# Performance work log

Hardware: AMD Instinct MI355X
Metric: run time of the kernel (lower is better)

## Reference

```python
import jax, jax.numpy as jnp
import numpy as np

NUM_LAYERS = 2


def _lstm_scan(x, w_ih, w_hh):
    """x: [S,B,I]; w_ih: [4H,I]; w_hh: [4H,H]. Returns per-step (hs, cs): [S,B,H]."""
    S, B, _ = x.shape
    H = w_hh.shape[1]
    xg = jnp.einsum('sbi,gi->sbg', x, w_ih)  # precompute input contributions [S,B,4H]

    def step(carry, xg_t):
        h, c = carry
        gates = xg_t + h @ w_hh.T
        i, f, g, o = jnp.split(gates, 4, axis=-1)  # torch LSTM gate order
        i = jax.nn.sigmoid(i)
        f = jax.nn.sigmoid(f)
        g = jnp.tanh(g)
        o = jax.nn.sigmoid(o)
        c = f * c + i * g
        h = o * jnp.tanh(c)
        return (h, c), (h, c)

    init = (jnp.zeros((B, H), x.dtype), jnp.zeros((B, H), x.dtype))
    _, (hs, cs) = jax.lax.scan(step, init, xg)
    return hs, cs


def _stacked(x, w_ih, w_hh, reverse):
    """Stacked unidirectional LSTM. w_ih/w_hh: [L,4H,*].
    Returns (out [S,B,H], h_last [L,B,H], c_last [L,B,H]) matching stackedRNN
    semantics: for reverse, the returned 'last' hidden is the per-step state at
    original time index S-1 (first step processed in the reverse loop)."""
    h_last, c_last = [], []
    cur = x
    for layer in range(w_ih.shape[0]):
        xin = jnp.flip(cur, axis=0) if reverse else cur
        hs, cs = _lstm_scan(xin, w_ih[layer], w_hh[layer])
        if reverse:
            hs = jnp.flip(hs, axis=0)
            cs = jnp.flip(cs, axis=0)
        cur = hs
        h_last.append(hs[-1])  # faithful to torch code's layer[-1] indexing
        c_last.append(cs[-1])
    return cur, jnp.stack(h_last, 0), jnp.stack(c_last, 0)


def setup_inputs() -> dict:
    key = jax.random.key(0)
    ks = jax.random.split(key, 5)
    S, B, I, H, L = 256, 32, 1024, 1024, NUM_LAYERS
    stdev = 1.0 / np.sqrt(H)
    u = lambda k, shape: jax.random.uniform(k, shape, jnp.float32, -stdev, stdev)
    return {
        'x': jax.random.normal(ks[0], (S, B, I), jnp.float32),
        'w_ih_fwd': u(ks[1], (L, 4 * H, I)),
        'w_hh_fwd': u(ks[2], (L, 4 * H, H)),
        'w_ih_bwd': u(ks[3], (L, 4 * H, I)),
        'w_hh_bwd': u(ks[4], (L, 4 * H, H)),
    }


def reference(x, w_ih_fwd, w_hh_fwd, w_ih_bwd, w_hh_bwd):
    out_f, h_f, c_f = _stacked(x, w_ih_fwd, w_hh_fwd, reverse=False)
    out_b, h_b, c_b = _stacked(x, w_ih_bwd, w_hh_bwd, reverse=True)
    output = jnp.concatenate([out_f, out_b], axis=-1)      # [S,B,2H]
    h_all = jnp.concatenate([h_f, h_b], axis=-1)            # [L,B,2H]
    c_all = jnp.concatenate([c_f, c_b], axis=-1)            # [L,B,2H]
    return output, h_all, c_all
```

## Files before the change

### kernel.cpp

```cpp
#include <hip/hip_runtime.h>
#include <stdint.h>

#define SEQ   256
#define BSZ   32
#define HD    1024
#define GD    4096
#define KD    1024
#define MROWS (SEQ*BSZ)
#define PBLK  256
#define PTHR  512

typedef unsigned short u16;
typedef __attribute__((ext_vector_type(8))) __bf16 bf8_t;
typedef __attribute__((ext_vector_type(4))) float  f4_t;
typedef __attribute__((ext_vector_type(4))) unsigned int u4_t;

__device__ __forceinline__ u16 f2bf(float f) {
  unsigned u = __float_as_uint(f);
  u += 0x7fffu + ((u >> 16) & 1u);
  return (u16)(u >> 16);
}
__device__ __forceinline__ float sigm(float x) { return 1.0f / (1.0f + __expf(-x)); }
__device__ __forceinline__ float tanh_f(float x) {
  float e = __expf(-2.0f * x);
  return 2.0f / (1.0f + e) - 1.0f;
}

__global__ void cvt_f32_bf16(const float* __restrict__ src, u16* __restrict__ dst, int n4) {
  int i = blockIdx.x * blockDim.x + threadIdx.x;
  if (i >= n4) return;
  float4 v = ((const float4*)src)[i];
  ushort4 o;
  o.x = f2bf(v.x); o.y = f2bf(v.y); o.z = f2bf(v.z); o.w = f2bf(v.w);
  ((ushort4*)dst)[i] = o;
}

__global__ void reorder_whh(const float* __restrict__ src, u16* __restrict__ dst, int d) {
  int r = blockIdx.x;
  int layer = r >> 12, row = r & 4095;
  int g = row >> 10, j = row & 1023;
  int jblk = j >> 4, jl = j & 15;
  size_t drow = ((size_t)(d * 2 + layer) * 64 + jblk) * 64 + g * 16 + jl;
  float4 v = ((const float4*)(src + (size_t)r * KD))[threadIdx.x];
  ushort4 o;
  o.x = f2bf(v.x); o.y = f2bf(v.y); o.z = f2bf(v.z); o.w = f2bf(v.w);
  ((ushort4*)(dst + drow * KD))[threadIdx.x] = o;
}

__global__ __launch_bounds__(PTHR, 2) void lstm_persist(
    const u16* __restrict__ whh_r,
    const u16* __restrict__ wih_r,
    const u16* __restrict__ xbf,
    u16*       __restrict__ h0t,
    u16*       __restrict__ h1t,
    float*     __restrict__ dout,
    unsigned*  __restrict__ cntb)
{
  const int tid = threadIdx.x;
  const int lane = tid & 63;
  const int wv  = tid >> 6;
  const int mt = wv >> 1, kh = wv & 1;
  const int bid = blockIdx.x;
  const int layer = bid >> 7;
  const int d = bid & 1, jblk = (bid >> 1) & 63;
  const int j0 = jblk * 16;
  const int fr = lane & 15, quad = lane >> 4;
  unsigned* cnt   = cntb + (size_t)(layer * 2 + d) * 512;
  unsigned* cntbl = cntb + (size_t)d * 512;

  __builtin_amdgcn_fence(__ATOMIC_ACQUIRE, "agent");

  __shared__ __align__(16) uint32_t lX[32 * 512];
  __shared__ __align__(16) uint32_t lH[32 * 512];
  __shared__ __align__(16) float lAcc[4096];

  u16*       hme = (layer ? h1t : h0t) + (size_t)d * MROWS * HD;
  const u16* hbl = h0t + (size_t)d * MROWS * HD;

  u4_t wih[16], whh[16];
  {
    const size_t rb = ((size_t)((d * 2 + layer) * 64 + jblk) * 64 + mt * 16 + fr) * KD
                    + kh * 512 + quad * 8;
    #pragma unroll
    for (int ks = 0; ks < 16; ks++) wih[ks] = *(const u4_t*)(wih_r + rb + ks * 32);
    #pragma unroll
    for (int ks = 0; ks < 16; ks++) whh[ks] = *(const u4_t*)(whh_r + rb + ks * 32);
    #pragma unroll
    for (int ks = 0; ks < 16; ks++) {
      asm volatile("" : "+v"(wih[ks]));
      asm volatile("" : "+v"(whh[ks]));
    }
  }

  const int b_ = tid >> 3, jp = tid & 7;
  float cr0 = 0.0f, cr1 = 0.0f;

  for (int t = 0; t < SEQ; t++) {
    const int tt = d ? (SEQ - 1 - t) : t;

    if (tid == 0) {
      const unsigned go = 8u * (unsigned)t;
      const unsigned gb = 8u * (unsigned)(t + 1);
      long spins = 0;
      for (;;) {
        bool ok = (__hip_atomic_load(&cnt[0], __ATOMIC_RELAXED, __HIP_MEMORY_SCOPE_AGENT) >= go);
        if (ok && layer)
          ok = (__hip_atomic_load(&cntbl[0], __ATOMIC_RELAXED, __HIP_MEMORY_SCOPE_AGENT) >= gb);
        if (ok) break;
        if (++spins > (1L << 22)) break;
      }
    }
    __syncthreads();
    asm volatile("" ::: "memory");

    if (wv < 4) {
      if (layer) {
        const unsigned long long* s8 = (const unsigned long long*)(hbl + (size_t)tt * BSZ * HD);
        #pragma unroll
        for (int hf = 0; hf < 2; hf++) {
          unsigned long long hv2[16];
          #pragma unroll
          for (int k = 0; k < 8; k++) {
            int kk = hf * 8 + k, row = wv * 8 + (kk >> 1), c = (kk & 1) * 64 + lane;
            size_t ci = ((size_t)row * 128 + c) * 2;
            hv2[2 * k]     = __hip_atomic_load(s8 + ci,     __ATOMIC_RELAXED, __HIP_MEMORY_SCOPE_AGENT);
            hv2[2 * k + 1] = __hip_atomic_load(s8 + ci + 1, __ATOMIC_RELAXED, __HIP_MEMORY_SCOPE_AGENT);
          }
          #pragma unroll
          for (int k = 0; k < 8; k++) {
            int kk = hf * 8 + k, row = wv * 8 + (kk >> 1), c = (kk & 1) * 64 + lane;
            int pc = c ^ (row & 7);
            uint2 lo = __builtin_bit_cast(uint2, hv2[2 * k]);
            uint2 hi = __builtin_bit_cast(uint2, hv2[2 * k + 1]);
            u4_t v; v.x = lo.x; v.y = lo.y; v.z = hi.x; v.w = hi.y;
            *(u4_t*)&lX[row * 512 + pc * 4] = v;
          }
        }
      } else if (t == 0) {
        const u16* xs = xbf + (size_t)(tt * BSZ) * KD;
        #pragma unroll
        for (int k = 0; k < 16; k++) {
          int row = wv * 8 + (k >> 1), c = (k & 1) * 64 + lane, pc = c ^ (row & 7);
          u4_t v = *(const u4_t*)(xs + (size_t)row * KD + c * 8);
          *(u4_t*)&lX[row * 512 + pc * 4] = v;
        }
      }
    } else if (t > 0) {
      const int q = wv - 4;
      const int ttp = d ? (tt + 1) : (tt - 1);
      const unsigned long long* s8 = (const unsigned long long*)(hme + (size_t)ttp * BSZ * HD);
      #pragma unroll
      for (int hf = 0; hf < 2; hf++) {
        unsigned long long hv2[16];
        #pragma unroll
        for (int k = 0; k < 8; k++) {
          int kk = hf * 8 + k, row = q * 8 + (kk >> 1), c = (kk & 1) * 64 + lane;
          size_t ci = ((size_t)row * 128 + c) * 2;
          hv2[2 * k]     = __hip_atomic_load(s8 + ci,     __ATOMIC_RELAXED, __HIP_MEMORY_SCOPE_AGENT);
          hv2[2 * k + 1] = __hip_atomic_load(s8 + ci + 1, __ATOMIC_RELAXED, __HIP_MEMORY_SCOPE_AGENT);
        }
        #pragma unroll
        for (int k = 0; k < 8; k++) {
          int kk = hf * 8 + k, row = q * 8 + (kk >> 1), c = (kk & 1) * 64 + lane;
          int pc = c ^ (row & 7);
          uint2 lo = __builtin_bit_cast(uint2, hv2[2 * k]);
          uint2 hi = __builtin_bit_cast(uint2, hv2[2 * k + 1]);
          u4_t v; v.x = lo.x; v.y = lo.y; v.z = hi.x; v.w = hi.y;
          *(u4_t*)&lH[row * 512 + pc * 4] = v;
        }
      }
    }
    __syncthreads();

    f4_t acc0 = {}, acc1 = {};
    #pragma unroll
    for (int ks = 0; ks < 16; ks++) {
      int cbase = ((kh * 64 + ks * 4 + quad) ^ (fr & 7)) << 2;
      bf8_t a0 = *(const bf8_t*)&lX[fr * 512 + cbase];
      bf8_t a1 = *(const bf8_t*)&lX[(fr + 16) * 512 + cbase];
      bf8_t wb = __builtin_bit_cast(bf8_t, wih[ks]);
      acc0 = __builtin_amdgcn_mfma_f32_16x16x32_bf16(a0, wb, acc0, 0, 0, 0);
      acc1 = __builtin_amdgcn_mfma_f32_16x16x32_bf16(a1, wb, acc1, 0, 0, 0);
    }
    if (t > 0) {
      #pragma unroll
      for (int ks = 0; ks < 16; ks++) {
        int cbase = ((kh * 64 + ks * 4 + quad) ^ (fr & 7)) << 2;
        bf8_t a0 = *(const bf8_t*)&lH[fr * 512 + cbase];
        bf8_t a1 = *(const bf8_t*)&lH[(fr + 16) * 512 + cbase];
        bf8_t wb = __builtin_bit_cast(bf8_t, whh[ks]);
        acc0 = __builtin_amdgcn_mfma_f32_16x16x32_bf16(a0, wb, acc0, 0, 0, 0);
        acc1 = __builtin_amdgcn_mfma_f32_16x16x32_bf16(a1, wb, acc1, 0, 0, 0);
      }
    }
    #pragma unroll
    for (int r = 0; r < 4; r++) {
      lAcc[((mt * 2 + kh) * 32 + quad * 4 + r) * 16 + fr]      = acc0[r];
      lAcc[((mt * 2 + kh) * 32 + 16 + quad * 4 + r) * 16 + fr] = acc1[r];
    }
    __syncthreads();

    if (tid < 256) {
      float vg0[4], vg1[4];
      #pragma unroll
      for (int g = 0; g < 4; g++) {
        float2 p0 = *(const float2*)&lAcc[((g * 2 + 0) * 32 + b_) * 16 + 2 * jp];
        float2 p1 = *(const float2*)&lAcc[((g * 2 + 1) * 32 + b_) * 16 + 2 * jp];
        vg0[g] = p0.x + p1.x;
        vg1[g] = p0.y + p1.y;
      }
      float i0 = sigm(vg0[0]), f0 = sigm(vg0[1]), g0 = tanh_f(vg0[2]), o0 = sigm(vg0[3]);
      float i1 = sigm(vg1[0]), f1 = sigm(vg1[1]), g1 = tanh_f(vg1[2]), o1 = sigm(vg1[3]);
      cr0 = f0 * cr0 + i0 * g0;
      cr1 = f1 * cr1 + i1 * g1;
      float hn0 = o0 * tanh_f(cr0), hn1 = o1 * tanh_f(cr1);
      uint32_t hnp = ((uint32_t)f2bf(hn1) << 16) | (uint32_t)f2bf(hn0);

      size_t hq = (((size_t)tt * BSZ + b_) * HD + j0 + 2 * jp) >> 1;
      __hip_atomic_store((uint32_t*)hme + hq, hnp, __ATOMIC_RELAXED, __HIP_MEMORY_SCOPE_AGENT);

      if (layer == 1) {
        float2 o2 = make_float2(hn0, hn1);
        *(float2*)&dout[((size_t)tt * BSZ + b_) * (2 * HD) + (size_t)d * HD + j0 + 2 * jp] = o2;
      }
      if ((d == 0 && t == SEQ - 1) || (d == 1 && t == 0)) {
        size_t hoff = (size_t)MROWS * 2 * HD + ((size_t)layer * BSZ + b_) * (2 * HD)
                    + (size_t)d * HD + j0 + 2 * jp;
        dout[hoff] = hn0;  dout[hoff + 1] = hn1;
        dout[hoff + (size_t)2 * BSZ * 2 * HD]     = cr0;
        dout[hoff + (size_t)2 * BSZ * 2 * HD + 1] = cr1;
      }
      asm volatile("s_waitcnt vmcnt(0)" ::: "memory");
    }

    if (!layer && wv < 4 && t + 1 < SEQ) {
      const int ttn = d ? (SEQ - 2 - t) : (t + 1);
      const u16* xs = xbf + (size_t)(ttn * BSZ) * KD;
      #pragma unroll
      for (int k = 0; k < 16; k++) {
        int row = wv * 8 + (k >> 1), c = (k & 1) * 64 + lane, pc = c ^ (row & 7);
        u4_t v = *(const u4_t*)(xs + (size_t)row * KD + c * 8);
        *(u4_t*)&lX[row * 512 + pc * 4] = v;
      }
    }

    __syncthreads();
    if (tid == 0) {
      const unsigned sub = (unsigned)(jblk & 7);
      unsigned old = __hip_atomic_fetch_add(&cnt[16 * (1 + sub)], 1u,
                                            __ATOMIC_RELAXED, __HIP_MEMORY_SCOPE_AGENT);
      if (old + 1u == 8u * (unsigned)(t + 1))
        __hip_atomic_fetch_add(&cnt[0], 1u, __ATOMIC_RELAXED, __HIP_MEMORY_SCOPE_AGENT);
    }
  }
}

extern "C" void kernel_launch(void* const* d_in, const int* in_sizes, int n_in,
                              void* d_out, int out_size, void* d_ws, size_t ws_size,
                              hipStream_t stream) {
  const float* x    = (const float*)d_in[0];
  const float* wihf = (const float*)d_in[1];
  const float* whhf = (const float*)d_in[2];
  const float* wihb = (const float*)d_in[3];
  const float* whhb = (const float*)d_in[4];
  float* out = (float*)d_out;

  const size_t NE = (size_t)MROWS * KD;
  u16* ws   = (u16*)d_ws;
  u16* xbf  = ws;
  u16* whhr = xbf + NE;
  u16* wihr = whhr + 2 * NE;
  u16* h0   = wihr + 2 * NE;
  u16* h1   = h0 + 2 * NE;
  unsigned* cnt = (unsigned*)(h1 + 2 * NE);

  const int n4 = (int)(NE / 4);
  cvt_f32_bf16<<<n4 / 256, 256, 0, stream>>>(x, xbf, n4);
  reorder_whh<<<2 * GD, 256, 0, stream>>>(whhf, whhr, 0);
  reorder_whh<<<2 * GD, 256, 0, stream>>>(whhb, whhr, 1);
  reorder_whh<<<2 * GD, 256, 0, stream>>>(wihf, wihr, 0);
  reorder_whh<<<2 * GD, 256, 0, stream>>>(wihb, wihr, 1);

  hipMemsetAsync(cnt, 0, 4 * 512 * sizeof(unsigned), stream);

  lstm_persist<<<PBLK, PTHR, 0, stream>>>(whhr, wihr, xbf, h0, h1, out, cnt);
}
```

Baseline: 3.027 ms.

## Prefetch layer-below hidden state for next step after signaling completion

Layer-1 blocks now wait on the layer-below counter and stage the next step's input hidden state into LDS at the end of the current step, after signaling completion. Before, that wait and load happened on the critical path at the start of each step. The barrier arrive and wait are moved to thread 256 (wave 4), so the waves doing the prefetch (0-3) are not the ones signaling. Hidden-state loads now use inline-asm global_load_dwordx4 with sc0 sc1 cache bits instead of paired 64-bit relaxed atomics. This trades a per-lane spin on the cross-layer counter for fewer serialized waits, and it relies on the cache-bypass bits for coherence.

```diff
diff --git a/kernel.cpp b/kernel.cpp
--- a/kernel.cpp
+++ b/kernel.cpp
@@ -24,6 +24,44 @@
 __device__ __forceinline__ float tanh_f(float x) {
   float e = __expf(-2.0f * x);
   return 2.0f / (1.0f + e) - 1.0f;
+}
+
+__device__ __forceinline__ u4_t load16_sc(const void* p) {
+  u4_t r;
+  asm volatile("global_load_dwordx4 %0, %1, off sc0 sc1"
+               : "=v"(r) : "v"(p));
+  return r;
+}
+
+__device__ __forceinline__ void stage_h64(const u16* src, uint32_t* lds,
+                                          int rbase, int lane) {
+  u4_t v[16];
+  #pragma unroll
+  for (int k = 0; k < 16; k++) {
+    int row = rbase + (k >> 1);
+    int c   = (k & 1) * 64 + lane;
+    v[k] = load16_sc(src + (size_t)row * 1024 + (size_t)c * 8);
+  }
+  asm volatile("s_waitcnt vmcnt(0)" ::: "memory");
+  #pragma unroll
+  for (int k = 0; k < 16; k++) {
+    int row = rbase + (k >> 1);
+    int c   = (k & 1) * 64 + lane;
+    int pc  = c ^ (row & 7);
+    *(u4_t*)&lds[row * 512 + pc * 4] = v[k];
+  }
+}
+
+__device__ __forceinline__ void stage_x64(const u16* src, uint32_t* lds,
+                                          int rbase, int lane) {
+  #pragma unroll
+  for (int k = 0; k < 16; k++) {
+    int row = rbase + (k >> 1);
+    int c   = (k & 1) * 64 + lane;
+    u4_t v  = *(const u4_t*)(src + (size_t)row * 1024 + (size_t)c * 8);
+    int pc  = c ^ (row & 7);
+    *(u4_t*)&lds[row * 512 + pc * 4] = v;
+  }
 }
 
 __global__ void cvt_f32_bf16(const float* __restrict__ src, u16* __restrict__ dst, int n4) {
@@ -98,14 +136,13 @@
   for (int t = 0; t < SEQ; t++) {
     const int tt = d ? (SEQ - 1 - t) : t;
 
-    if (tid == 0) {
+    if (tid == 256) {
       const unsigned go = 8u * (unsigned)t;
-      const unsigned gb = 8u * (unsigned)(t + 1);
       long spins = 0;
       for (;;) {
         bool ok = (__hip_atomic_load(&cnt[0], __ATOMIC_RELAXED, __HIP_MEMORY_SCOPE_AGENT) >= go);
-        if (ok && layer)
-          ok = (__hip_atomic_load(&cntbl[0], __ATOMIC_RELAXED, __HIP_MEMORY_SCOPE_AGENT) >= gb);
+        if (ok && layer && t == 0)
+          ok = (__hip_atomic_load(&cntbl[0], __ATOMIC_RELAXED, __HIP_MEMORY_SCOPE_AGENT) >= 8u);
         if (ok) break;
         if (++spins > (1L << 22)) break;
       }
@@ -113,62 +150,14 @@
     __syncthreads();
     asm volatile("" ::: "memory");
 
-    if (wv < 4) {
-      if (layer) {
-        const unsigned long long* s8 = (const unsigned long long*)(hbl + (size_t)tt * BSZ * HD);
-        #pragma unroll
-        for (int hf = 0; hf < 2; hf++) {
-          unsigned long long hv2[16];
-          #pragma unroll
-          for (int k = 0; k < 8; k++) {
-            int kk = hf * 8 + k, row = wv * 8 + (kk >> 1), c = (kk & 1) * 64 + lane;
-            size_t ci = ((size_t)row * 128 + c) * 2;
-            hv2[2 * k]     = __hip_atomic_load(s8 + ci,     __ATOMIC_RELAXED, __HIP_MEMORY_SCOPE_AGENT);
-            hv2[2 * k + 1] = __hip_atomic_load(s8 + ci + 1, __ATOMIC_RELAXED, __HIP_MEMORY_SCOPE_AGENT);
-          }
-          #pragma unroll
-          for (int k = 0; k < 8; k++) {
-            int kk = hf * 8 + k, row = wv * 8 + (kk >> 1), c = (kk & 1) * 64 + lane;
-            int pc = c ^ (row & 7);
-            uint2 lo = __builtin_bit_cast(uint2, hv2[2 * k]);
-            uint2 hi = __builtin_bit_cast(uint2, hv2[2 * k + 1]);
-            u4_t v; v.x = lo.x; v.y = lo.y; v.z = hi.x; v.w = hi.y;
-            *(u4_t*)&lX[row * 512 + pc * 4] = v;
-          }
-        }
-      } else if (t == 0) {
-        const u16* xs = xbf + (size_t)(tt * BSZ) * KD;
-        #pragma unroll
-        for (int k = 0; k < 16; k++) {
-          int row = wv * 8 + (k >> 1), c = (k & 1) * 64 + lane, pc = c ^ (row & 7);
-          u4_t v = *(const u4_t*)(xs + (size_t)row * KD + c * 8);
-          *(u4_t*)&lX[row * 512 + pc * 4] = v;
-        }
-      }
-    } else if (t > 0) {
-      const int q = wv - 4;
-      const int ttp = d ? (tt + 1) : (tt - 1);
-      const unsigned long long* s8 = (const unsigned long long*)(hme + (size_t)ttp * BSZ * HD);
-      #pragma unroll
-      for (int hf = 0; hf < 2; hf++) {
-        unsigned long long hv2[16];
-        #pragma unroll
-        for (int k = 0; k < 8; k++) {
-          int kk = hf * 8 + k, row = q * 8 + (kk >> 1), c = (kk & 1) * 64 + lane;
-          size_t ci = ((size_t)row * 128 + c) * 2;
-          hv2[2 * k]     = __hip_atomic_load(s8 + ci,     __ATOMIC_RELAXED, __HIP_MEMORY_SCOPE_AGENT);
-          hv2[2 * k + 1] = __hip_atomic_load(s8 + ci + 1, __ATOMIC_RELAXED, __HIP_MEMORY_SCOPE_AGENT);
-        }
-        #pragma unroll
-        for (int k = 0; k < 8; k++) {
-          int kk = hf * 8 + k, row = q * 8 + (kk >> 1), c = (kk & 1) * 64 + lane;
-          int pc = c ^ (row & 7);
-          uint2 lo = __builtin_bit_cast(uint2, hv2[2 * k]);
-          uint2 hi = __builtin_bit_cast(uint2, hv2[2 * k + 1]);
-          u4_t v; v.x = lo.x; v.y = lo.y; v.z = hi.x; v.w = hi.y;
-          *(u4_t*)&lH[row * 512 + pc * 4] = v;
-        }
-      }
+    if (t > 0) {
+      if (wv >= 4) {
+        const int ttp = d ? (tt + 1) : (tt - 1);
+        stage_h64(hme + (size_t)ttp * BSZ * HD, lH, (wv - 4) * 8, lane);
+      }
+    } else if (wv < 4) {
+      if (layer) stage_h64(hbl + (size_t)tt * BSZ * HD, lX, wv * 8, lane);
+      else       stage_x64(xbf + (size_t)(tt * BSZ) * KD, lX, wv * 8, lane);
     }
     __syncthreads();
 
@@ -233,24 +222,28 @@
       asm volatile("s_waitcnt vmcnt(0)" ::: "memory");
     }
 
-    if (!layer && wv < 4 && t + 1 < SEQ) {
-      const int ttn = d ? (SEQ - 2 - t) : (t + 1);
-      const u16* xs = xbf + (size_t)(ttn * BSZ) * KD;
-      #pragma unroll
-      for (int k = 0; k < 16; k++) {
-        int row = wv * 8 + (k >> 1), c = (k & 1) * 64 + lane, pc = c ^ (row & 7);
-        u4_t v = *(const u4_t*)(xs + (size_t)row * KD + c * 8);
-        *(u4_t*)&lX[row * 512 + pc * 4] = v;
-      }
-    }
-
-    __syncthreads();
-    if (tid == 0) {
+    __syncthreads();
+
+    if (tid == 256) {
       const unsigned sub = (unsigned)(jblk & 7);
       unsigned old = __hip_atomic_fetch_add(&cnt[16 * (1 + sub)], 1u,
                                             __ATOMIC_RELAXED, __HIP_MEMORY_SCOPE_AGENT);
       if (old + 1u == 8u * (unsigned)(t + 1))
         __hip_atomic_fetch_add(&cnt[0], 1u, __ATOMIC_RELAXED, __HIP_MEMORY_SCOPE_AGENT);
+    }
+    if (wv < 4 && t + 1 < SEQ) {
+      const int ttn = d ? (SEQ - 2 - t) : (t + 1);
+      if (layer) {
+        long spins = 0;
+        while (__hip_atomic_load(&cntbl[0], __ATOMIC_RELAXED, __HIP_MEMORY_SCOPE_AGENT)
+               < 8u * (unsigned)(t + 2)) {
+          if (++spins > (1L << 22)) break;
+        }
+        asm volatile("" ::: "memory");
+        stage_h64(hbl + (size_t)ttn * BSZ * HD, lX, wv * 8, lane);
+      } else {
+        stage_x64(xbf + (size_t)(ttn * BSZ) * KD, lX, wv * 8, lane);
+      }
     }
   }
 }
```

Measured after the change: 3.081 ms. About the same (+1.8%).
